# Kernel optimization log

Hardware: AMD Instinct MI355X
Metric: run time of the kernel (lower is better)

## Reference

```python
import jax, jax.numpy as jnp
import numpy as np

NV, NK, DK, DV, KC = 32, 16, 128, 128, 4  # value heads, key heads, head dims, conv kernel
EPS = 1e-6


def setup_inputs() -> dict:
    key = jax.random.key(0)
    ks = jax.random.split(key, 10)
    B, T, D = 2, 4096, 2048
    key_dim, value_dim = NK * DK, NV * DV
    conv_dim = 2 * key_dim + value_dim
    s = 0.02
    return {
        "hidden_states": jax.random.normal(ks[0], (B, T, D), jnp.float32),
        "W_qkv": jax.random.normal(ks[1], (D, conv_dim), jnp.float32) * s,
        "W_z": jax.random.normal(ks[2], (D, value_dim), jnp.float32) * s,
        "W_b": jax.random.normal(ks[3], (D, NV), jnp.float32) * s,
        "W_a": jax.random.normal(ks[4], (D, NV), jnp.float32) * s,
        "conv_w": jax.random.normal(ks[5], (conv_dim, KC), jnp.float32) * 0.2,
        "dt_bias": jnp.ones((NV,), jnp.float32),
        "A_log": jnp.log(jax.random.uniform(ks[6], (NV,), jnp.float32, 0.5, 16.0)),
        "norm_w": jnp.ones((DV,), jnp.float32),
        "W_out": jax.random.normal(ks[7], (value_dim, D), jnp.float32) * s,
    }


def _silu(x):
    return x * jax.nn.sigmoid(x)


def _l2norm(x):
    return x * jax.lax.rsqrt(jnp.sum(x * x, axis=-1, keepdims=True) + EPS)


def _gated_delta_rule(q, k, v, g, beta):
    # q,k: [B,T,H,DK]; v: [B,T,H,DV]; g,beta: [B,T,H]
    tm = lambda x: jnp.moveaxis(x, 1, 0)  # time-major
    B, T, H = q.shape[0], q.shape[1], q.shape[2]
    S0 = jnp.zeros((B, H, q.shape[-1], v.shape[-1]), q.dtype)

    def step(S, xs):
        qt, kt, vt, gt, bt = xs
        S = S * jnp.exp(gt)[..., None, None]                       # decay
        kS = jnp.einsum('bhk,bhkv->bhv', kt, S)                    # k^T S
        S = S + bt[..., None, None] * kt[..., :, None] * (vt - kS)[..., None, :]
        o = jnp.einsum('bhk,bhkv->bhv', qt, S)
        return S, o

    _, o = jax.lax.scan(step, S0, (tm(q), tm(k), tm(v), tm(g), tm(beta)))
    return jnp.moveaxis(o, 0, 1)  # [B,T,H,DV]


def reference(hidden_states, W_qkv, W_z, W_b, W_a, conv_w, dt_bias, A_log, norm_w, W_out):
    B, T, D = hidden_states.shape
    key_dim, value_dim = NK * DK, NV * DV

    mixed = hidden_states @ W_qkv                                  # [B,T,conv_dim]
    z = (hidden_states @ W_z).reshape(B, T, NV, DV)
    beta = jax.nn.sigmoid(hidden_states @ W_b)                     # [B,T,NV]
    a = hidden_states @ W_a
    g = -jnp.exp(A_log) * jax.nn.softplus(a + dt_bias)             # [B,T,NV]

    # causal depthwise short conv (kernel KC) + silu
    xp = jnp.pad(mixed, ((0, 0), (KC - 1, 0), (0, 0)))
    conv = sum(xp[:, i:i + T, :] * conv_w[:, i] for i in range(KC))
    mixed = _silu(conv)

    q, k, v = jnp.split(mixed, [key_dim, 2 * key_dim], axis=-1)
    q = q.reshape(B, T, NK, DK)
    k = k.reshape(B, T, NK, DK)
    v = v.reshape(B, T, NV, DV)
    rep = NV // NK
    q = jnp.repeat(q, rep, axis=2)
    k = jnp.repeat(k, rep, axis=2)

    q = _l2norm(q) * (DK ** -0.5)
    k = _l2norm(k)

    o = _gated_delta_rule(q, k, v, g, beta)                        # [B,T,NV,DV]

    # fused gated RMSNorm: rmsnorm(o)*w * silu(z)
    var = jnp.mean(o * o, axis=-1, keepdims=True)
    o = o * jax.lax.rsqrt(var + 1e-6) * norm_w * _silu(z)

    return o.reshape(B, T, value_dim) @ W_out
```

## Files before the change

kernel.cpp:

```cpp
#include <hip/hip_runtime.h>
#include <hip/hip_bf16.h>


typedef __attribute__((ext_vector_type(8))) short short8;
typedef __attribute__((ext_vector_type(4))) float f32x4;
typedef unsigned short us;

static __device__ __forceinline__ us f2b(float f) {
  __hip_bfloat16 h = __float2bfloat16(f);
  return __builtin_bit_cast(us, h);
}
static __device__ __forceinline__ float b2f(us u) {
  return __bfloat162float(__builtin_bit_cast(__hip_bfloat16, u));
}

__global__ __launch_bounds__(256) void cvt_f32_bf16(const float* __restrict__ in,
    us* __restrict__ out, long n4) {
  long i = (long)blockIdx.x * 256 + threadIdx.x;
  long stride = (long)gridDim.x * 256;
  for (; i < n4; i += stride) {
    float4 f = reinterpret_cast<const float4*>(in)[i];
    ushort4 u;
    u.x = f2b(f.x); u.y = f2b(f.y); u.z = f2b(f.z); u.w = f2b(f.w);
    reinterpret_cast<ushort4*>(out)[i] = u;
  }
}

__global__ __launch_bounds__(256) void transpose_cvt(const float* __restrict__ in,
    us* __restrict__ out, int K, int N, int Nfull, int coloff, int row_off) {
  __shared__ float tile[32][33];
  int tx = threadIdx.x & 31, ty = threadIdx.x >> 5;
  int n0 = blockIdx.x * 32, k0 = blockIdx.y * 32;
#pragma unroll
  for (int r = 0; r < 4; ++r) {
    int kk = k0 + ty + r * 8, nn = n0 + tx;
    tile[ty + r * 8][tx] = (kk < K && nn < N) ? in[(size_t)kk * Nfull + coloff + nn] : 0.f;
  }
  __syncthreads();
#pragma unroll
  for (int r = 0; r < 4; ++r) {
    int nn = n0 + ty + r * 8, kk = k0 + tx;
    if (nn < N && kk < K)
      out[(size_t)(nn + row_off) * K + kk] = f2b(tile[tx][ty + r * 8]);
  }
}

template <bool BF16OUT>
__global__ __launch_bounds__(512, 1) void gemm256(const us* __restrict__ A,
    const us* __restrict__ B, void* __restrict__ Cout, int K, int ldC) {
  __shared__ us Abuf[2][256 * 64];
  __shared__ us Bbuf[2][256 * 64];
  int tid = threadIdx.x, w = tid >> 6, lane = tid & 63;
  int wr = w >> 2, wc = w & 3;
  int fr = lane & 15, j4 = lane >> 4;
  int lin = blockIdx.y * gridDim.x + blockIdx.x;
  int nwg = gridDim.x * gridDim.y;
  int wg = (lin & 7) * (nwg >> 3) + (lin >> 3);
  int bx = wg % gridDim.x, by = wg / gridDim.x;
  size_t bm = (size_t)bx * 256, bn = (size_t)by * 256;

  const us *aG[4], *bG[4];
  us *aL[2][4], *bL[2][4];
#pragma unroll
  for (int u = 0; u < 4; ++u) {
    int idx = u * 512 + tid;
    int row = idx >> 3, sl = idx & 7;
    int sg = (sl ^ (row & 7)) * 8;
    aG[u] = A + (bm + row) * K + sg;
    bG[u] = B + (bn + row) * K + sg;
    int lbase = (u * 64 + w * 8) * 64;
#pragma unroll
    for (int bf = 0; bf < 2; ++bf) {
      aL[bf][u] = &Abuf[bf][lbase];
      bL[bf][u] = &Bbuf[bf][lbase];
    }
  }

  f32x4 acc[8][4] = {};
#pragma unroll
  for (int u = 0; u < 4; ++u) {
    __builtin_amdgcn_global_load_lds((const void*)aG[u], (void*)aL[0][u], 16, 0, 0);
    __builtin_amdgcn_global_load_lds((const void*)bG[u], (void*)bL[0][u], 16, 0, 0);
  }
  __syncthreads();

  int nt = K >> 6;
  for (int t = 0; t < nt; ++t) {
    int cur = t & 1, nxt = cur ^ 1;
    const us* Ac = Abuf[cur];
    const us* Bc = Bbuf[cur];
    int kt1 = (t + 1) << 6;
    bool more = (t + 1 < nt);
#pragma unroll
    for (int q = 0; q < 4; ++q) {
      if (more) {
        __builtin_amdgcn_global_load_lds((const void*)(aG[q] + kt1), (void*)aL[nxt][q], 16, 0, 0);
        __builtin_amdgcn_global_load_lds((const void*)(bG[q] + kt1), (void*)bL[nxt][q], 16, 0, 0);
      }
      short8 a0[2], a1[2], bfv[4][2];
      int Ra0 = wr * 128 + 2 * q * 16 + fr;
      int Ra1 = Ra0 + 16;
#pragma unroll
      for (int ks = 0; ks < 2; ++ks) {
        a0[ks] = *reinterpret_cast<const short8*>(&Ac[Ra0 * 64 + (((ks * 4 + j4) ^ (Ra0 & 7)) * 8)]);
        a1[ks] = *reinterpret_cast<const short8*>(&Ac[Ra1 * 64 + (((ks * 4 + j4) ^ (Ra1 & 7)) * 8)]);
#pragma unroll
        for (int fj = 0; fj < 4; ++fj) {
          int Rb = wc * 64 + fj * 16 + fr;
          bfv[fj][ks] = *reinterpret_cast<const short8*>(&Bc[Rb * 64 + (((ks * 4 + j4) ^ (Rb & 7)) * 8)]);
        }
      }
      __builtin_amdgcn_s_setprio(1);
#pragma unroll
      for (int ks = 0; ks < 2; ++ks)
#pragma unroll
        for (int fj = 0; fj < 4; ++fj) {
          acc[2 * q][fj] = __builtin_amdgcn_mfma_f32_16x16x32_bf16(a0[ks], bfv[fj][ks], acc[2 * q][fj], 0, 0, 0);
          acc[2 * q + 1][fj] = __builtin_amdgcn_mfma_f32_16x16x32_bf16(a1[ks], bfv[fj][ks], acc[2 * q + 1][fj], 0, 0, 0);
        }
      __builtin_amdgcn_s_setprio(0);
    }
    __syncthreads();
  }
#pragma unroll
  for (int fi = 0; fi < 8; ++fi)
#pragma unroll
    for (int fj = 0; fj < 4; ++fj) {
      size_t col = bn + wc * 64 + fj * 16 + fr;
#pragma unroll
      for (int e = 0; e < 4; ++e) {
        size_t r = bm + wr * 128 + fi * 16 + j4 * 4 + e;
        size_t off = r * ldC + col;
        if (BF16OUT) reinterpret_cast<us*>(Cout)[off] = f2b(acc[fi][fj][e]);
        else reinterpret_cast<float*>(Cout)[off] = acc[fi][fj][e];
      }
    }
}

__global__ __launch_bounds__(256) void gemm_lds_f32(const us* __restrict__ A,
    const us* __restrict__ B, float* __restrict__ Cout,
    int K, int Nb1, int Nvalid, int ldC) {
  __shared__ us Ash[128 * 64];
  __shared__ us Bsh[128 * 64];
  int tid = threadIdx.x, w = tid >> 6, lane = tid & 63;
  int bm = blockIdx.x * 128, bn = blockIdx.y * 128;
  int wm = (w >> 1) * 64, wn = (w & 1) * 64;
  const us* aP[4]; const us* bP[4]; us* lA[4]; us* lB[4];
#pragma unroll
  for (int i = 0; i < 4; ++i) {
    int idx = i * 256 + tid;
    int row = idx >> 3;
    int sg = ((idx & 7) ^ (row & 7)) * 8;
    aP[i] = A + (size_t)(bm + row) * K + sg;
    int rb = bn + row; if (rb > Nb1) rb = Nb1;
    bP[i] = B + (size_t)rb * K + sg;
    lA[i] = &Ash[(i * 256 + w * 64) * 8];
    lB[i] = &Bsh[(i * 256 + w * 64) * 8];
  }
  f32x4 acc[4][4] = {};
  int fr = lane & 15, j = lane >> 4;
  for (int kt = 0; kt < K; kt += 64) {
#pragma unroll
    for (int i = 0; i < 4; ++i)
      __builtin_amdgcn_global_load_lds((const void*)(aP[i] + kt), (void*)lA[i], 16, 0, 0);
#pragma unroll
    for (int i = 0; i < 4; ++i)
      __builtin_amdgcn_global_load_lds((const void*)(bP[i] + kt), (void*)lB[i], 16, 0, 0);
    __syncthreads();
#pragma unroll
    for (int ks = 0; ks < 2; ++ks) {
      short8 af[4], bfr[4];
#pragma unroll
      for (int f = 0; f < 4; ++f) {
        int Ra = wm + f * 16 + fr;
        af[f] = *reinterpret_cast<const short8*>(&Ash[Ra * 64 + (((ks * 4 + j) ^ (Ra & 7)) * 8)]);
        int Rb = wn + f * 16 + fr;
        bfr[f] = *reinterpret_cast<const short8*>(&Bsh[Rb * 64 + (((ks * 4 + j) ^ (Rb & 7)) * 8)]);
      }
#pragma unroll
      for (int i = 0; i < 4; ++i)
#pragma unroll
        for (int jj = 0; jj < 4; ++jj)
          acc[i][jj] = __builtin_amdgcn_mfma_f32_16x16x32_bf16(af[i], bfr[jj], acc[i][jj], 0, 0, 0);
    }
    __syncthreads();
  }
#pragma unroll
  for (int i = 0; i < 4; ++i)
#pragma unroll
    for (int jj = 0; jj < 4; ++jj) {
      int c0 = bn + wn + jj * 16 + (lane & 15);
      if (c0 < Nvalid) {
#pragma unroll
        for (int e = 0; e < 4; ++e) {
          int r = bm + wm + i * 16 + (lane >> 4) * 4 + e;
          Cout[(size_t)r * ldC + c0] = acc[i][jj][e];
        }
      }
    }
}

template <int MODE>
__global__ __launch_bounds__(256) void conv_chunk(const us* __restrict__ mixed,
    const float* __restrict__ cw, us* __restrict__ outp, int headbase) {
  int bt = blockIdx.x, b = bt >> 12, t = bt & 4095, tid = threadIdx.x;
  float x[8];
#pragma unroll
  for (int jj = 0; jj < 8; ++jj) {
    int c = jj * 256 + tid;
    float4 w4 = *reinterpret_cast<const float4*>(cw + (size_t)c * 4);
    float wv[4] = {w4.x, w4.y, w4.z, w4.w};
    float acc = 0.f;
#pragma unroll
    for (int i = 0; i < 4; ++i) {
      int tt = t - 3 + i;
      if (tt >= 0) acc += b2f(mixed[((size_t)(b * 4096 + tt)) * 2048 + c]) * wv[i];
    }
    x[jj] = acc / (1.f + __expf(-acc));
  }
  if (MODE < 2) {
    __shared__ float wsum[4][8];
    int wid = tid >> 6;
#pragma unroll
    for (int jj = 0; jj < 8; ++jj) {
      float s2 = x[jj] * x[jj];
#pragma unroll
      for (int m = 1; m < 64; m <<= 1) s2 += __shfl_xor(s2, m, 64);
      if ((tid & 63) == 0) wsum[wid][jj] = s2;
    }
    __syncthreads();
#pragma unroll
    for (int jj = 0; jj < 8; ++jj) {
      int w0 = (tid >> 7) * 2;
      float rn = rsqrtf(wsum[w0][jj] + wsum[w0 + 1][jj] + 1e-6f);
      int c = jj * 256 + tid;
      float val = x[jj] * rn * (MODE == 0 ? 0.08838834764831845f : 1.f);
      outp[((size_t)bt * 16 + (c >> 7)) * 128 + (c & 127)] = f2b(val);
    }
  } else {
#pragma unroll
    for (int jj = 0; jj < 8; ++jj) {
      int c = jj * 256 + tid;
      outp[((size_t)bt * 32 + headbase + (c >> 7)) * 128 + (c & 127)] = f2b(x[jj]);
    }
  }
}

__global__ __launch_bounds__(256) void gates_cumsum(const float* __restrict__ ba,
    const float* __restrict__ dt_bias, const float* __restrict__ A_log,
    float* __restrict__ bl_g, float* __restrict__ beta_g) {
  int widx = blockIdx.x * 4 + (threadIdx.x >> 6);
  int lane = threadIdx.x & 63;
  int bh = widx >> 6, chunk = widx & 63;
  int b = bh >> 5, h = bh & 31;
  size_t btl = (size_t)b * 4096 + chunk * 64 + lane;
  float bv = ba[btl * 64 + h];
  float av = ba[btl * 64 + 32 + h];
  float beta = 1.f / (1.f + __expf(-bv));
  float xx = av + dt_bias[h];
  float sp = (xx > 20.f) ? xx : log1pf(__expf(xx));
  float g = -__expf(A_log[h]) * sp;
#pragma unroll
  for (int off = 1; off < 64; off <<= 1) {
    float n = __shfl_up(g, off, 64);
    if (lane >= off) g += n;
  }
  bl_g[(size_t)widx * 64 + lane] = g;
  beta_g[(size_t)widx * 64 + lane] = beta;
}

static __device__ __forceinline__ f32x4 tile_range(const us* A, int lda,
    const us* B, int ldb, int rt, int ct, int l0, int nk, int lane, f32x4 acc) {
  const us* ar = A + (rt * 16 + (lane & 15)) * lda + l0 * 16 + (lane >> 4) * 8;
  const us* br = B + (ct * 16 + (lane & 15)) * ldb + l0 * 16 + (lane >> 4) * 8;
#pragma unroll
  for (int ks = 0; ks < nk; ++ks) {
    short8 a = *reinterpret_cast<const short8*>(ar + ks * 32);
    short8 bb = *reinterpret_cast<const short8*>(br + ks * 32);
    acc = __builtin_amdgcn_mfma_f32_16x16x32_bf16(a, bb, acc, 0, 0, 0);
  }
  return acc;
}

__global__ __launch_bounds__(512, 1) void scan_p1(
    const us* __restrict__ k, const float* __restrict__ bl_g,
    const float* __restrict__ beta_g, us* __restrict__ Tg) {
  __shared__ us Kb[64 * 136];
  __shared__ us Ebt[64 * 72];
  __shared__ us W1[64 * 72], W1t[64 * 72], W3[64 * 72];
  __shared__ float bl_s[64], bet_s[64];
  us* const Eb = Kb;

  int bid = blockIdx.x, bh = bid >> 6, c = bid & 63;
  int b = bh >> 5, h = bh & 31, hk = h >> 1;
  int tid = threadIdx.x, w = tid >> 6, lane = tid & 63;
  int row = tid >> 3, c16 = (tid & 7) * 16;
  size_t bt0 = (size_t)b * 4096 + c * 64;

  const int TR_[10] = {0, 1, 1, 2, 2, 2, 3, 3, 3, 3};
  const int TC_[10] = {0, 0, 1, 0, 1, 2, 0, 1, 2, 3};

  const us* kp = k + ((bt0 + row) * 16 + hk) * 128 + c16;
  uint4 kr0 = reinterpret_cast<const uint4*>(kp)[0];
  uint4 kr1 = reinterpret_cast<const uint4*>(kp)[1];
  int gbase = (bh * 64 + c) * 64;
  if (tid < 64) { bl_s[tid] = bl_g[gbase + tid]; bet_s[tid] = beta_g[gbase + tid]; }
  *reinterpret_cast<uint4*>(&Kb[row * 136 + c16]) = kr0;
  *reinterpret_cast<uint4*>(&Kb[row * 136 + c16 + 8]) = kr1;
  __syncthreads();
  {
    int art = w & 3;
#pragma unroll
    for (int s = 0; s < 2; ++s) {
      int ct = (w >> 2) * 2 + s;
      f32x4 a = tile_range(Kb, 136, Kb, 136, art, ct, 0, 4, lane, f32x4{});
#pragma unroll
      for (int e = 0; e < 4; ++e) {
        int tr = art * 16 + (lane >> 4) * 4 + e;
        int cl = ct * 16 + (lane & 15);
        float dv = (cl < tr) ? bet_s[tr] * __expf(bl_s[tr] - bl_s[cl]) * a[e] : 0.f;
        W1[tr * 72 + cl] = f2b(dv);
        W1t[cl * 72 + tr] = f2b(dv);
        W3[tr * 72 + cl] = f2b((tr == cl ? 1.f : 0.f) - dv);
      }
    }
  }
  __syncthreads();
  f32x4 freg[2] = {};
#pragma unroll
  for (int it = 1; it <= 5; ++it) {
    if (it > 1) {
#pragma unroll
      for (int s = 0; s < 2; ++s) {
        int j = w + s * 8;
        if (j < 10) {
          int r = TR_[j], cc0 = TC_[j];
#pragma unroll
          for (int e = 0; e < 4; ++e) {
            int rr = r * 16 + (lane >> 4) * 4 + e, cl = cc0 * 16 + (lane & 15);
            W3[rr * 72 + cl] = f2b(b2f(W3[rr * 72 + cl]) + freg[s][e]);
          }
        }
      }
    }
    if (it == 1) {
      const int ZR[12] = {0, 0, 0, 1, 1, 2, 1, 2, 2, 3, 3, 3};
      const int ZC[12] = {1, 2, 3, 2, 3, 3, 0, 0, 1, 0, 1, 2};
#pragma unroll
      for (int u = 0; u < 12; ++u) {
        if ((u & 7) != w) continue;
        us* arr = (u < 6) ? Eb : Ebt;
        if (lane < 32) {
          int rr = ZR[u] * 16 + (lane >> 1);
          *reinterpret_cast<uint4*>(&arr[rr * 72 + ZC[u] * 16 + (lane & 1) * 8]) =
              make_uint4(0, 0, 0, 0);
        }
      }
    }
    const us* Es  = (it & 1) ? W1  : Eb;
    const us* Est = (it & 1) ? W1t : Ebt;
    us* Ed  = (it & 1) ? Eb  : W1;
    us* Edt = (it & 1) ? Ebt : W1t;
#pragma unroll
    for (int s = 0; s < 2; ++s) {
      int j = w + s * 8;
      if (j < 10) {
        int r = TR_[j], cc0 = TC_[j];
        int l0 = cc0 & ~1, nk = (r - l0 + 2) >> 1;
        f32x4 a = tile_range(Es, 72, Est, 72, r, cc0, l0, nk, lane, f32x4{});
#pragma unroll
        for (int e = 0; e < 4; ++e) {
          int rr = r * 16 + (lane >> 4) * 4 + e, cl = cc0 * 16 + (lane & 15);
          us val = f2b(a[e]);
          Ed[rr * 72 + cl] = val;
          Edt[cl * 72 + rr] = val;
        }
      }
    }
    __syncthreads();
    const us* Ent = (it & 1) ? Ebt : W1t;
#pragma unroll
    for (int s = 0; s < 2; ++s) {
      int j = w + s * 8;
      if (j < 10) {
        int r = TR_[j], cc0 = TC_[j];
        int l0 = cc0 & ~1, nk = (r - l0 + 2) >> 1;
        freg[s] = tile_range(W3, 72, Ent, 72, r, cc0, l0, nk, lane, f32x4{});
      }
    }
    __syncthreads();
  }
#pragma unroll
  for (int s = 0; s < 2; ++s) {
    int j = w + s * 8;
    if (j < 10) {
      int r = TR_[j], cc0 = TC_[j];
#pragma unroll
      for (int e = 0; e < 4; ++e) {
        int rr = r * 16 + (lane >> 4) * 4 + e, cl = cc0 * 16 + (lane & 15);
        W3[rr * 72 + cl] = f2b(b2f(W3[rr * 72 + cl]) + freg[s][e]);
      }
    }
  }
  __syncthreads();
  *reinterpret_cast<uint4*>(&Tg[(size_t)bid * 4096 + tid * 8]) =
      *reinterpret_cast<const uint4*>(&W3[row * 72 + (tid & 7) * 8]);
}

__global__ __launch_bounds__(512, 1) void scan_p2(
    const us* __restrict__ q, const us* __restrict__ k, const us* __restrict__ v,
    const float* __restrict__ bl_g, const float* __restrict__ beta_g,
    const us* __restrict__ Tg, us* __restrict__ o) {
  __shared__ us Sb[32 * 136];
  __shared__ us Kb[64 * 136];
  __shared__ us Qb[64 * 136];
  __shared__ us Ktb[128 * 72];
  __shared__ us Vt[32 * 72];
  __shared__ us Ut[32 * 72];
  __shared__ us W3[64 * 72];
  __shared__ us WP[64 * 72];
  __shared__ float bl_s[64], bet_s[64];

  int bid = blockIdx.x, vs = bid >> 6, bh = bid & 63;
  int b = bh >> 5, h = bh & 31, hk = h >> 1;
  int tid = threadIdx.x, w = tid >> 6, lane = tid & 63;
  int row = tid >> 3, c16 = (tid & 7) * 16;

  for (int i = tid; i < (32 * 136) / 8; i += 512)
    reinterpret_cast<uint4*>(Sb)[i] = make_uint4(0, 0, 0, 0);
  __syncthreads();

  uint4 kr0, kr1, qr0, qr1, vr, Tr;
  float blr, blC, bet, betv;
  int vrow = (tid & 255) >> 2, vseg = tid & 3;
  auto load_regs = [&](int c) {
    size_t bt0 = (size_t)b * 4096 + c * 64;
    const us* kp = k + ((bt0 + row) * 16 + hk) * 128 + c16;
    const us* qp = q + ((bt0 + row) * 16 + hk) * 128 + c16;
    kr0 = reinterpret_cast<const uint4*>(kp)[0];
    kr1 = reinterpret_cast<const uint4*>(kp)[1];
    qr0 = reinterpret_cast<const uint4*>(qp)[0];
    qr1 = reinterpret_cast<const uint4*>(qp)[1];
    Tr = *reinterpret_cast<const uint4*>(&Tg[((size_t)bh * 64 + c) * 4096 + tid * 8]);
    int gbase = (bh * 64 + c) * 64;
    blr = bl_g[gbase + row];
    blC = bl_g[gbase + 63];
    bet = beta_g[gbase + row];
    if (tid < 256) {
      vr = *reinterpret_cast<const uint4*>(
          v + ((bt0 + vrow) * 32 + h) * 128 + vs * 32 + vseg * 8);
      betv = beta_g[gbase + vrow];
    }
  };
  load_regs(0);

  for (int c = 0; c < 64; ++c) {
    size_t bt0 = (size_t)b * 4096 + c * 64;
    if ((tid & 7) == 0) { bl_s[row] = blr; bet_s[row] = bet; }
    *reinterpret_cast<uint4*>(&Kb[row * 136 + c16]) = kr0;
    *reinterpret_cast<uint4*>(&Kb[row * 136 + c16 + 8]) = kr1;
    *reinterpret_cast<uint4*>(&Qb[row * 136 + c16]) = qr0;
    *reinterpret_cast<uint4*>(&Qb[row * 136 + c16 + 8]) = qr1;
    *reinterpret_cast<uint4*>(&W3[row * 72 + (tid & 7) * 8]) = Tr;
    {
      us kreg[16];
      *reinterpret_cast<uint4*>(kreg) = kr0; *reinterpret_cast<uint4*>(kreg + 8) = kr1;
      float ksc = __expf(blC - blr);
#pragma unroll
      for (int i = 0; i < 16; ++i) Ktb[(c16 + i) * 72 + row] = f2b(ksc * b2f(kreg[i]));
    }
    if (tid < 256) {
      us vreg[8];
      *reinterpret_cast<uint4*>(vreg) = vr;
#pragma unroll
      for (int i = 0; i < 8; ++i) Vt[(vseg * 8 + i) * 72 + vrow] = f2b(betv * b2f(vreg[i]));
    }
    load_regs(c < 63 ? c + 1 : 63);
    __syncthreads();
    int rtO = w >> 1, ctv = w & 1;
    f32x4 o1 = tile_range(Qb, 136, Sb, 136, rtO, ctv, 0, 4, lane, f32x4{});
    {
      int art = w & 3;
#pragma unroll
      for (int s = 0; s < 2; ++s) {
        int ct = (w >> 2) * 2 + s;
        f32x4 a = tile_range(Qb, 136, Kb, 136, art, ct, 0, 4, lane, f32x4{});
#pragma unroll
        for (int e = 0; e < 4; ++e) {
          int tr = art * 16 + (lane >> 4) * 4 + e;
          int cl = ct * 16 + (lane & 15);
          float pv = (cl <= tr) ? __expf(bl_s[tr] - bl_s[cl]) * a[e] : 0.f;
          WP[tr * 72 + cl] = f2b(pv);
        }
      }
    }
    {
      int vrt = w >> 2, ct = w & 3;
      f32x4 a = tile_range(Sb, 136, Kb, 136, vrt, ct, 0, 4, lane, f32x4{});
      int tt = ct * 16 + (lane & 15);
      float csc = bet_s[tt] * __expf(bl_s[tt]);
#pragma unroll
      for (int e = 0; e < 4; ++e) {
        int vv = vrt * 16 + (lane >> 4) * 4 + e;
        Vt[vv * 72 + tt] = f2b(b2f(Vt[vv * 72 + tt]) - csc * a[e]);
      }
    }
    __syncthreads();
    {
      int vrt = w >> 2, ct = w & 3;
      f32x4 a = tile_range(Vt, 72, W3, 72, vrt, ct, 0, 2, lane, f32x4{});
#pragma unroll
      for (int e = 0; e < 4; ++e)
        Ut[(vrt * 16 + (lane >> 4) * 4 + e) * 72 + ct * 16 + (lane & 15)] = f2b(a[e]);
    }
    __syncthreads();
    float lamC = __expf(bl_s[63]);
    {
      f32x4 a = tile_range(WP, 72, Ut, 72, rtO, ctv, 0, 2, lane, f32x4{});
#pragma unroll
      for (int e = 0; e < 4; ++e) {
        int tt = rtO * 16 + (lane >> 4) * 4 + e;
        int vv = vs * 32 + ctv * 16 + (lane & 15);
        float val = __expf(bl_s[tt]) * o1[e] + a[e];
        o[((bt0 + tt) * 32 + h) * 128 + vv] = f2b(val);
      }
    }
#pragma unroll
    for (int s = 0; s < 2; ++s) {
      int ti = w * 2 + s;
      int vrt = ti >> 3, dt = ti & 7;
      f32x4 a = tile_range(Ut, 72, Ktb, 72, vrt, dt, 0, 2, lane, f32x4{});
#pragma unroll
      for (int e = 0; e < 4; ++e) {
        int vv = vrt * 16 + (lane >> 4) * 4 + e, dd = dt * 16 + (lane & 15);
        Sb[vv * 136 + dd] = f2b(lamC * b2f(Sb[vv * 136 + dd]) + a[e]);
      }
    }
    __syncthreads();
  }
}

__global__ __launch_bounds__(256) void rms_gate(us* oy,
    const us* __restrict__ z, const float* __restrict__ nw) {
  int wid = threadIdx.x >> 6, lane = threadIdx.x & 63;
  size_t base = ((size_t)blockIdx.x * 4 + wid) * 128;
  float o0 = b2f(oy[base + lane]), o1 = b2f(oy[base + lane + 64]);
  float ss = o0 * o0 + o1 * o1;
#pragma unroll
  for (int m = 1; m < 64; m <<= 1) ss += __shfl_xor(ss, m, 64);
  float r = rsqrtf(ss * (1.f / 128.f) + 1e-6f);
  float z0 = b2f(z[base + lane]), z1 = b2f(z[base + lane + 64]);
  z0 = z0 / (1.f + __expf(-z0));
  z1 = z1 / (1.f + __expf(-z1));
  oy[base + lane] = f2b(o0 * r * nw[lane] * z0);
  oy[base + lane + 64] = f2b(o1 * r * nw[lane + 64] * z1);
}

extern "C" void kernel_launch(void* const* d_in, const int* in_sizes, int n_in,
                              void* d_out, int out_size, void* d_ws, size_t ws_size,
                              hipStream_t stream) {
  const float* hs      = (const float*)d_in[0];
  const float* W_qkv   = (const float*)d_in[1];
  const float* W_z     = (const float*)d_in[2];
  const float* W_b     = (const float*)d_in[3];
  const float* W_a     = (const float*)d_in[4];
  const float* conv_w  = (const float*)d_in[5];
  const float* dt_bias = (const float*)d_in[6];
  const float* A_log   = (const float*)d_in[7];
  const float* norm_w  = (const float*)d_in[8];
  const float* W_out   = (const float*)d_in[9];
  float* out = (float*)d_out;

  char* ws = (char*)d_ws;
  const size_t MiB = 1u << 20;
  float* ba_buf = (float*)(ws);
  float* bl_g   = (float*)(ws + 2 * MiB);
  float* bt_g   = (float*)(ws + 3 * MiB);
  us*    wt     = (us*)(ws + 4 * MiB);
  us*    Tg     = (us*)(ws + 4 * MiB);
  us*    mixed  = (us*)(ws + 36 * MiB);
  us*    o_buf  = (us*)(ws + 36 * MiB);
  us*    hs_bf0 = (us*)(ws + 68 * MiB);
  us*    q_buf  = (us*)(ws + 100 * MiB);
  us*    hs_bf1 = q_buf;
  us*    k_buf  = (us*)(ws + 132 * MiB);
  us*    v_buf  = (us*)(ws + 164 * MiB);
  us*    z_bf   = v_buf;

  cvt_f32_bf16<<<2048, 256, 0, stream>>>(hs, hs_bf0, (long)8192 * 2048 / 4);

  for (int c = 0; c < 4; ++c) {
    transpose_cvt<<<dim3(64, 64), 256, 0, stream>>>(W_qkv, wt, 2048, 2048, 8192, c * 2048, 0);
    gemm256<true><<<dim3(32, 8), 512, 0, stream>>>(hs_bf0, wt, mixed, 2048, 2048);
    const float* cwc = conv_w + (size_t)c * 2048 * 4;
    if (c == 0)      conv_chunk<0><<<8192, 256, 0, stream>>>(mixed, cwc, q_buf, 0);
    else if (c == 1) conv_chunk<1><<<8192, 256, 0, stream>>>(mixed, cwc, k_buf, 0);
    else if (c == 2) conv_chunk<2><<<8192, 256, 0, stream>>>(mixed, cwc, v_buf, 0);
    else             conv_chunk<2><<<8192, 256, 0, stream>>>(mixed, cwc, v_buf, 16);
  }
  transpose_cvt<<<dim3(1, 64), 256, 0, stream>>>(W_b, wt, 2048, 32, 32, 0, 0);
  transpose_cvt<<<dim3(1, 64), 256, 0, stream>>>(W_a, wt, 2048, 32, 32, 0, 32);
  gemm_lds_f32<<<dim3(64, 1), 256, 0, stream>>>(hs_bf0, wt, ba_buf, 2048, 63, 64, 64);
  gates_cumsum<<<1024, 256, 0, stream>>>(ba_buf, dt_bias, A_log, bl_g, bt_g);
  scan_p1<<<4096, 512, 0, stream>>>(k_buf, bl_g, bt_g, Tg);
  scan_p2<<<256, 512, 0, stream>>>(q_buf, k_buf, v_buf, bl_g, bt_g, Tg, o_buf);
  cvt_f32_bf16<<<2048, 256, 0, stream>>>(hs, hs_bf1, (long)8192 * 2048 / 4);
  transpose_cvt<<<dim3(128, 64), 256, 0, stream>>>(W_z, wt, 2048, 4096, 4096, 0, 0);
  gemm256<true><<<dim3(32, 16), 512, 0, stream>>>(hs_bf1, wt, z_bf, 2048, 4096);
  rms_gate<<<65536, 256, 0, stream>>>(o_buf, z_bf, norm_w);
  transpose_cvt<<<dim3(64, 128), 256, 0, stream>>>(W_out, wt, 4096, 2048, 2048, 0, 0);
  gemm256<false><<<dim3(32, 8), 512, 0, stream>>>(o_buf, wt, out, 4096, 2048);
}
```

Baseline: 1.225 ms.

## Vectorize transpose, conv, rms_gate and split GEMM prefetch barriers

```diff
diff --git a/kernel.cpp b/kernel.cpp
--- a/kernel.cpp
+++ b/kernel.cpp
@@ -28,20 +28,33 @@
 
 __global__ __launch_bounds__(256) void transpose_cvt(const float* __restrict__ in,
     us* __restrict__ out, int K, int N, int Nfull, int coloff, int row_off) {
-  __shared__ float tile[32][33];
-  int tx = threadIdx.x & 31, ty = threadIdx.x >> 5;
-  int n0 = blockIdx.x * 32, k0 = blockIdx.y * 32;
+  __shared__ float tile[64][65];
+  int tid = threadIdx.x;
+  int n0 = blockIdx.x * 64, k0 = blockIdx.y * 64;
+  int tx = tid & 15, ty = tid >> 4;
 #pragma unroll
   for (int r = 0; r < 4; ++r) {
-    int kk = k0 + ty + r * 8, nn = n0 + tx;
-    tile[ty + r * 8][tx] = (kk < K && nn < N) ? in[(size_t)kk * Nfull + coloff + nn] : 0.f;
+    int kk = k0 + ty + r * 16, nn = n0 + tx * 4;
+    float4 v = make_float4(0.f, 0.f, 0.f, 0.f);
+    if (kk < K && nn < N)
+      v = *reinterpret_cast<const float4*>(in + (size_t)kk * Nfull + coloff + nn);
+    tile[ty + r * 16][tx * 4 + 0] = v.x;
+    tile[ty + r * 16][tx * 4 + 1] = v.y;
+    tile[ty + r * 16][tx * 4 + 2] = v.z;
+    tile[ty + r * 16][tx * 4 + 3] = v.w;
   }
   __syncthreads();
 #pragma unroll
-  for (int r = 0; r < 4; ++r) {
-    int nn = n0 + ty + r * 8, kk = k0 + tx;
-    if (nn < N && kk < K)
-      out[(size_t)(nn + row_off) * K + kk] = f2b(tile[tx][ty + r * 8]);
+  for (int g = 0; g < 2; ++g) {
+    int s = tid + g * 256;
+    int nn = s >> 3, ks = (s & 7) * 8;
+    if (n0 + nn < N && k0 + ks < K) {
+      us ov[8];
+#pragma unroll
+      for (int i = 0; i < 8; ++i) ov[i] = f2b(tile[ks + i][nn]);
+      *reinterpret_cast<uint4*>(out + (size_t)(n0 + nn + row_off) * K + k0 + ks) =
+          *reinterpret_cast<uint4*>(ov);
+    }
   }
 }
 
@@ -77,12 +90,14 @@
   }
 
   f32x4 acc[8][4] = {};
-#pragma unroll
-  for (int u = 0; u < 4; ++u) {
-    __builtin_amdgcn_global_load_lds((const void*)aG[u], (void*)aL[0][u], 16, 0, 0);
-    __builtin_amdgcn_global_load_lds((const void*)bG[u], (void*)bL[0][u], 16, 0, 0);
-  }
-  __syncthreads();
+  __builtin_amdgcn_global_load_lds((const void*)aG[0], (void*)aL[0][0], 16, 0, 0);
+  __builtin_amdgcn_global_load_lds((const void*)aG[2], (void*)aL[0][2], 16, 0, 0);
+  __builtin_amdgcn_global_load_lds((const void*)bG[0], (void*)bL[0][0], 16, 0, 0);
+  __builtin_amdgcn_global_load_lds((const void*)bG[1], (void*)bL[0][1], 16, 0, 0);
+  __builtin_amdgcn_global_load_lds((const void*)bG[2], (void*)bL[0][2], 16, 0, 0);
+  __builtin_amdgcn_global_load_lds((const void*)bG[3], (void*)bL[0][3], 16, 0, 0);
+  __builtin_amdgcn_global_load_lds((const void*)aG[1], (void*)aL[0][1], 16, 0, 0);
+  __builtin_amdgcn_global_load_lds((const void*)aG[3], (void*)aL[0][3], 16, 0, 0);
 
   int nt = K >> 6;
   for (int t = 0; t < nt; ++t) {
@@ -91,19 +106,39 @@
     const us* Bc = Bbuf[cur];
     int kt1 = (t + 1) << 6;
     bool more = (t + 1 < nt);
+    asm volatile("s_waitcnt vmcnt(2)" ::: "memory");
+    __builtin_amdgcn_s_barrier();
+    __builtin_amdgcn_sched_barrier(0);
 #pragma unroll
     for (int q = 0; q < 4; ++q) {
+      if (q == 2) {
+        if (more) { asm volatile("s_waitcnt vmcnt(4)" ::: "memory"); }
+        else      { asm volatile("s_waitcnt vmcnt(0)" ::: "memory"); }
+        __builtin_amdgcn_s_barrier();
+        __builtin_amdgcn_sched_barrier(0);
+      }
       if (more) {
-        __builtin_amdgcn_global_load_lds((const void*)(aG[q] + kt1), (void*)aL[nxt][q], 16, 0, 0);
-        __builtin_amdgcn_global_load_lds((const void*)(bG[q] + kt1), (void*)bL[nxt][q], 16, 0, 0);
-      }
-      short8 a0[2], a1[2], bfv[4][2];
+        if (q == 0) {
+          __builtin_amdgcn_global_load_lds((const void*)(aG[0] + kt1), (void*)aL[nxt][0], 16, 0, 0);
+          __builtin_amdgcn_global_load_lds((const void*)(aG[2] + kt1), (void*)aL[nxt][2], 16, 0, 0);
+        } else if (q == 1) {
+          __builtin_amdgcn_global_load_lds((const void*)(bG[0] + kt1), (void*)bL[nxt][0], 16, 0, 0);
+          __builtin_amdgcn_global_load_lds((const void*)(bG[1] + kt1), (void*)bL[nxt][1], 16, 0, 0);
+        } else if (q == 2) {
+          __builtin_amdgcn_global_load_lds((const void*)(bG[2] + kt1), (void*)bL[nxt][2], 16, 0, 0);
+          __builtin_amdgcn_global_load_lds((const void*)(bG[3] + kt1), (void*)bL[nxt][3], 16, 0, 0);
+        } else {
+          __builtin_amdgcn_global_load_lds((const void*)(aG[1] + kt1), (void*)aL[nxt][1], 16, 0, 0);
+          __builtin_amdgcn_global_load_lds((const void*)(aG[3] + kt1), (void*)aL[nxt][3], 16, 0, 0);
+        }
+      }
+      short8 a0v[2], a1v[2], bfv[4][2];
       int Ra0 = wr * 128 + 2 * q * 16 + fr;
       int Ra1 = Ra0 + 16;
 #pragma unroll
       for (int ks = 0; ks < 2; ++ks) {
-        a0[ks] = *reinterpret_cast<const short8*>(&Ac[Ra0 * 64 + (((ks * 4 + j4) ^ (Ra0 & 7)) * 8)]);
-        a1[ks] = *reinterpret_cast<const short8*>(&Ac[Ra1 * 64 + (((ks * 4 + j4) ^ (Ra1 & 7)) * 8)]);
+        a0v[ks] = *reinterpret_cast<const short8*>(&Ac[Ra0 * 64 + (((ks * 4 + j4) ^ (Ra0 & 7)) * 8)]);
+        a1v[ks] = *reinterpret_cast<const short8*>(&Ac[Ra1 * 64 + (((ks * 4 + j4) ^ (Ra1 & 7)) * 8)]);
 #pragma unroll
         for (int fj = 0; fj < 4; ++fj) {
           int Rb = wc * 64 + fj * 16 + fr;
@@ -115,12 +150,11 @@
       for (int ks = 0; ks < 2; ++ks)
 #pragma unroll
         for (int fj = 0; fj < 4; ++fj) {
-          acc[2 * q][fj] = __builtin_amdgcn_mfma_f32_16x16x32_bf16(a0[ks], bfv[fj][ks], acc[2 * q][fj], 0, 0, 0);
-          acc[2 * q + 1][fj] = __builtin_amdgcn_mfma_f32_16x16x32_bf16(a1[ks], bfv[fj][ks], acc[2 * q + 1][fj], 0, 0, 0);
+          acc[2 * q][fj] = __builtin_amdgcn_mfma_f32_16x16x32_bf16(a0v[ks], bfv[fj][ks], acc[2 * q][fj], 0, 0, 0);
+          acc[2 * q + 1][fj] = __builtin_amdgcn_mfma_f32_16x16x32_bf16(a1v[ks], bfv[fj][ks], acc[2 * q + 1][fj], 0, 0, 0);
         }
       __builtin_amdgcn_s_setprio(0);
     }
-    __syncthreads();
   }
 #pragma unroll
   for (int fi = 0; fi < 8; ++fi)
@@ -204,45 +238,46 @@
 __global__ __launch_bounds__(256) void conv_chunk(const us* __restrict__ mixed,
     const float* __restrict__ cw, us* __restrict__ outp, int headbase) {
   int bt = blockIdx.x, b = bt >> 12, t = bt & 4095, tid = threadIdx.x;
+  int c0 = tid * 8;
+  float wv[8][4];
+#pragma unroll
+  for (int jj = 0; jj < 8; ++jj) {
+    float4 w4 = *reinterpret_cast<const float4*>(cw + (size_t)(c0 + jj) * 4);
+    wv[jj][0] = w4.x; wv[jj][1] = w4.y; wv[jj][2] = w4.z; wv[jj][3] = w4.w;
+  }
+  float acc[8] = {};
+#pragma unroll
+  for (int i = 0; i < 4; ++i) {
+    int tt = t - 3 + i;
+    if (tt >= 0) {
+      us r[8];
+      *reinterpret_cast<uint4*>(r) = *reinterpret_cast<const uint4*>(
+          mixed + ((size_t)(b * 4096 + tt)) * 2048 + c0);
+#pragma unroll
+      for (int jj = 0; jj < 8; ++jj) acc[jj] += b2f(r[jj]) * wv[jj][i];
+    }
+  }
   float x[8];
 #pragma unroll
-  for (int jj = 0; jj < 8; ++jj) {
-    int c = jj * 256 + tid;
-    float4 w4 = *reinterpret_cast<const float4*>(cw + (size_t)c * 4);
-    float wv[4] = {w4.x, w4.y, w4.z, w4.w};
-    float acc = 0.f;
-#pragma unroll
-    for (int i = 0; i < 4; ++i) {
-      int tt = t - 3 + i;
-      if (tt >= 0) acc += b2f(mixed[((size_t)(b * 4096 + tt)) * 2048 + c]) * wv[i];
-    }
-    x[jj] = acc / (1.f + __expf(-acc));
-  }
+  for (int jj = 0; jj < 8; ++jj) x[jj] = acc[jj] / (1.f + __expf(-acc[jj]));
+  us ov[8];
   if (MODE < 2) {
-    __shared__ float wsum[4][8];
-    int wid = tid >> 6;
-#pragma unroll
-    for (int jj = 0; jj < 8; ++jj) {
-      float s2 = x[jj] * x[jj];
-#pragma unroll
-      for (int m = 1; m < 64; m <<= 1) s2 += __shfl_xor(s2, m, 64);
-      if ((tid & 63) == 0) wsum[wid][jj] = s2;
-    }
-    __syncthreads();
-#pragma unroll
-    for (int jj = 0; jj < 8; ++jj) {
-      int w0 = (tid >> 7) * 2;
-      float rn = rsqrtf(wsum[w0][jj] + wsum[w0 + 1][jj] + 1e-6f);
-      int c = jj * 256 + tid;
-      float val = x[jj] * rn * (MODE == 0 ? 0.08838834764831845f : 1.f);
-      outp[((size_t)bt * 16 + (c >> 7)) * 128 + (c & 127)] = f2b(val);
-    }
+    float s2 = 0.f;
+#pragma unroll
+    for (int jj = 0; jj < 8; ++jj) s2 += x[jj] * x[jj];
+#pragma unroll
+    for (int m = 1; m < 16; m <<= 1) s2 += __shfl_xor(s2, m, 64);
+    float rn = rsqrtf(s2 + 1e-6f) * (MODE == 0 ? 0.08838834764831845f : 1.f);
+#pragma unroll
+    for (int jj = 0; jj < 8; ++jj) ov[jj] = f2b(x[jj] * rn);
+    int head = tid >> 4, d0 = c0 & 127;
+    *reinterpret_cast<uint4*>(outp + ((size_t)bt * 16 + head) * 128 + d0) =
+        *reinterpret_cast<uint4*>(ov);
   } else {
 #pragma unroll
-    for (int jj = 0; jj < 8; ++jj) {
-      int c = jj * 256 + tid;
-      outp[((size_t)bt * 32 + headbase + (c >> 7)) * 128 + (c & 127)] = f2b(x[jj]);
-    }
+    for (int jj = 0; jj < 8; ++jj) ov[jj] = f2b(x[jj]);
+    *reinterpret_cast<uint4*>(outp + ((size_t)bt * 32 + headbase + (c0 >> 7)) * 128 + (c0 & 127)) =
+        *reinterpret_cast<uint4*>(ov);
   }
 }
 
@@ -542,18 +577,26 @@
 
 __global__ __launch_bounds__(256) void rms_gate(us* oy,
     const us* __restrict__ z, const float* __restrict__ nw) {
-  int wid = threadIdx.x >> 6, lane = threadIdx.x & 63;
-  size_t base = ((size_t)blockIdx.x * 4 + wid) * 128;
-  float o0 = b2f(oy[base + lane]), o1 = b2f(oy[base + lane + 64]);
-  float ss = o0 * o0 + o1 * o1;
-#pragma unroll
-  for (int m = 1; m < 64; m <<= 1) ss += __shfl_xor(ss, m, 64);
+  int sub = threadIdx.x & 31;
+  size_t row = (size_t)blockIdx.x * 8 + (threadIdx.x >> 5);
+  size_t base = row * 128 + sub * 4;
+  ushort4 ov = *reinterpret_cast<ushort4*>(oy + base);
+  ushort4 zv = *reinterpret_cast<const ushort4*>(z + base);
+  float o_[4] = {b2f(ov.x), b2f(ov.y), b2f(ov.z), b2f(ov.w)};
+  float ss = o_[0] * o_[0] + o_[1] * o_[1] + o_[2] * o_[2] + o_[3] * o_[3];
+#pragma unroll
+  for (int m = 1; m < 32; m <<= 1) ss += __shfl_xor(ss, m, 64);
   float r = rsqrtf(ss * (1.f / 128.f) + 1e-6f);
-  float z0 = b2f(z[base + lane]), z1 = b2f(z[base + lane + 64]);
-  z0 = z0 / (1.f + __expf(-z0));
-  z1 = z1 / (1.f + __expf(-z1));
-  oy[base + lane] = f2b(o0 * r * nw[lane] * z0);
-  oy[base + lane + 64] = f2b(o1 * r * nw[lane + 64] * z1);
+  float4 w4 = *reinterpret_cast<const float4*>(nw + sub * 4);
+  float zz[4] = {b2f(zv.x), b2f(zv.y), b2f(zv.z), b2f(zv.w)};
+  float wv[4] = {w4.x, w4.y, w4.z, w4.w};
+  us res[4];
+#pragma unroll
+  for (int i = 0; i < 4; ++i) {
+    float zs = zz[i] / (1.f + __expf(-zz[i]));
+    res[i] = f2b(o_[i] * r * wv[i] * zs);
+  }
+  *reinterpret_cast<ushort4*>(oy + base) = *reinterpret_cast<ushort4*>(res);
 }
 
 extern "C" void kernel_launch(void* const* d_in, const int* in_sizes, int n_in,
@@ -590,7 +633,7 @@
   cvt_f32_bf16<<<2048, 256, 0, stream>>>(hs, hs_bf0, (long)8192 * 2048 / 4);
 
   for (int c = 0; c < 4; ++c) {
-    transpose_cvt<<<dim3(64, 64), 256, 0, stream>>>(W_qkv, wt, 2048, 2048, 8192, c * 2048, 0);
+    transpose_cvt<<<dim3(32, 32), 256, 0, stream>>>(W_qkv, wt, 2048, 2048, 8192, c * 2048, 0);
     gemm256<true><<<dim3(32, 8), 512, 0, stream>>>(hs_bf0, wt, mixed, 2048, 2048);
     const float* cwc = conv_w + (size_t)c * 2048 * 4;
     if (c == 0)      conv_chunk<0><<<8192, 256, 0, stream>>>(mixed, cwc, q_buf, 0);
@@ -598,16 +641,16 @@
     else if (c == 2) conv_chunk<2><<<8192, 256, 0, stream>>>(mixed, cwc, v_buf, 0);
     else             conv_chunk<2><<<8192, 256, 0, stream>>>(mixed, cwc, v_buf, 16);
   }
-  transpose_cvt<<<dim3(1, 64), 256, 0, stream>>>(W_b, wt, 2048, 32, 32, 0, 0);
-  transpose_cvt<<<dim3(1, 64), 256, 0, stream>>>(W_a, wt, 2048, 32, 32, 0, 32);
+  transpose_cvt<<<dim3(1, 32), 256, 0, stream>>>(W_b, wt, 2048, 32, 32, 0, 0);
+  transpose_cvt<<<dim3(1, 32), 256, 0, stream>>>(W_a, wt, 2048, 32, 32, 0, 32);
   gemm_lds_f32<<<dim3(64, 1), 256, 0, stream>>>(hs_bf0, wt, ba_buf, 2048, 63, 64, 64);
   gates_cumsum<<<1024, 256, 0, stream>>>(ba_buf, dt_bias, A_log, bl_g, bt_g);
   scan_p1<<<4096, 512, 0, stream>>>(k_buf, bl_g, bt_g, Tg);
   scan_p2<<<256, 512, 0, stream>>>(q_buf, k_buf, v_buf, bl_g, bt_g, Tg, o_buf);
   cvt_f32_bf16<<<2048, 256, 0, stream>>>(hs, hs_bf1, (long)8192 * 2048 / 4);
-  transpose_cvt<<<dim3(128, 64), 256, 0, stream>>>(W_z, wt, 2048, 4096, 4096, 0, 0);
+  transpose_cvt<<<dim3(64, 32), 256, 0, stream>>>(W_z, wt, 2048, 4096, 4096, 0, 0);
   gemm256<true><<<dim3(32, 16), 512, 0, stream>>>(hs_bf1, wt, z_bf, 2048, 4096);
-  rms_gate<<<65536, 256, 0, stream>>>(o_buf, z_bf, norm_w);
-  transpose_cvt<<<dim3(64, 128), 256, 0, stream>>>(W_out, wt, 4096, 2048, 2048, 0, 0);
+  rms_gate<<<32768, 256, 0, stream>>>(o_buf, z_bf, norm_w);
+  transpose_cvt<<<dim3(32, 64), 256, 0, stream>>>(W_out, wt, 4096, 2048, 2048, 0, 0);
   gemm256<false><<<dim3(32, 8), 512, 0, stream>>>(o_buf, wt, out, 4096, 2048);
 }
```

Result: slower. 1.306 ms (+6.6%).
